# Performance work log

Hardware: AMD Instinct MI355X
Metric: run time of the kernel (lower is better)

## Reference

```python
import jax, jax.numpy as jnp
import numpy as np

STRIDE = 1
MAX_STRIDE = 250  # 25 * 10 default


def setup_inputs() -> dict:
    key = jax.random.key(0)
    k1, k2 = jax.random.split(key)
    T = 1_000_000
    prediction = jax.random.normal(k1, (T,), dtype=jnp.float32)
    ground_truth = jax.random.normal(k2, (T,), dtype=jnp.float32)
    return {"prediction": prediction, "ground_truth": ground_truth}


def reference(prediction, ground_truth):
    T = prediction.shape[0]
    lags = jnp.arange(0, MAX_STRIDE, STRIDE)
    idx = jnp.arange(T)

    # ground-truth statistics are lag-independent
    mean_gt = jnp.mean(ground_truth)
    var_gt = jnp.var(ground_truth, ddof=1)  # torch.var is unbiased
    v_gt = ground_truth - mean_gt

    def ccc_at_lag(n):
        # shifted pred: n leading zeros followed by prediction[:-n]
        src = idx - n
        pred = jnp.where(src >= 0, prediction[jnp.clip(src, 0)], 0.0)
        mean_pred = jnp.mean(pred)
        var_pred = jnp.var(pred, ddof=1)
        cov = jnp.mean((pred - mean_pred) * v_gt)  # population covariance
        denom = var_gt + var_pred + (mean_gt - mean_pred) ** 2
        return 2.0 * cov / denom

    cccs = jax.vmap(ccc_at_lag)(lags)  # [n_lags]
    return 1.0 - jnp.mean(cccs)
```

## Files before the change

kernel.cpp:

```cpp
#include <hip/hip_runtime.h>
#include <hip/hip_bf16.h>


#define TC 2048
#define NLAG 256
#define NUSED 250
#define GT4 (TC / 4 + 66)
#define STATS_OFF (512 * NLAG)
#define STATS_PITCH 512

__device__ __forceinline__ float4 ld_gt_sw(const float* s_gt, int i4) {
    int s = i4 ^ ((i4 >> 3) & 7);
    return *(const float4*)&s_gt[4 * s];
}

__global__ __launch_bounds__(256) void ccc_main(const float* __restrict__ pred,
                                                const float* __restrict__ gt,
                                                float* __restrict__ ws, int T) {
    __shared__ __align__(16) float s_pred[TC];
    __shared__ __align__(16) float s_gt[GT4 * 4];
    __shared__ __align__(16) float s_acc[8][NLAG];
    __shared__ float s_red[4][4];

    const int tid = threadIdx.x;
    const int c = blockIdx.x;
    const int j0 = c * TC;

    float sp = 0.f, qp = 0.f, sg = 0.f, qg = 0.f;
    #pragma unroll 2
    for (int i4 = tid; i4 < TC / 4; i4 += 256) {
        int g = j0 + 4 * i4;
        float4 v = make_float4(0.f, 0.f, 0.f, 0.f);
        if (g + 3 < T) v = *(const float4*)&pred[g];
        *(float4*)&s_pred[4 * i4] = v;
        sp += v.x + v.y + v.z + v.w;
        qp += v.x * v.x + v.y * v.y + v.z * v.z + v.w * v.w;
    }
    #pragma unroll 2
    for (int i4 = tid; i4 < GT4; i4 += 256) {
        int g = j0 + 4 * i4;
        float4 v = make_float4(0.f, 0.f, 0.f, 0.f);
        if (g + 3 < T) v = *(const float4*)&gt[g];
        int s = i4 ^ ((i4 >> 3) & 7);
        *(float4*)&s_gt[4 * s] = v;
        if (i4 < TC / 4) {
            sg += v.x + v.y + v.z + v.w;
            qg += v.x * v.x + v.y * v.y + v.z * v.z + v.w * v.w;
        }
    }
    __syncthreads();

    const int sub = tid >> 5;
    const int l = tid & 31;
    int gi = sub * 64 + 2 * l;
    const int pi0 = sub * 64;

    float w[12];
    {
        float4 a = ld_gt_sw(s_gt, gi);
        float4 b = ld_gt_sw(s_gt, gi + 1);
        float4 d = ld_gt_sw(s_gt, gi + 2);
        w[0] = a.x; w[1] = a.y; w[2] = a.z; w[3] = a.w;
        w[4] = b.x; w[5] = b.y; w[6] = b.z; w[7] = b.w;
        w[8] = d.x; w[9] = d.y; w[10] = d.z; w[11] = d.w;
    }
    float acc[8] = {0.f, 0.f, 0.f, 0.f, 0.f, 0.f, 0.f, 0.f};

    #pragma unroll 4
    for (int it = 0; it < 64; ++it) {
        float4 nw = ld_gt_sw(s_gt, gi + 3 + it);
        float4 p = *(const float4*)&s_pred[4 * (pi0 + it)];
        #pragma unroll
        for (int k = 0; k < 8; ++k) {
            acc[k] = fmaf(p.x, w[k], acc[k]);
            acc[k] = fmaf(p.y, w[k + 1], acc[k]);
            acc[k] = fmaf(p.z, w[k + 2], acc[k]);
            acc[k] = fmaf(p.w, w[k + 3], acc[k]);
        }
        #pragma unroll
        for (int i = 0; i < 8; ++i) w[i] = w[i + 4];
        w[8] = nw.x; w[9] = nw.y; w[10] = nw.z; w[11] = nw.w;
    }

    const int wv = tid >> 6, ln = tid & 63;
    #pragma unroll
    for (int off = 32; off > 0; off >>= 1) {
        sp += __shfl_down(sp, off, 64);
        qp += __shfl_down(qp, off, 64);
        sg += __shfl_down(sg, off, 64);
        qg += __shfl_down(qg, off, 64);
    }
    if (ln == 0) { s_red[wv][0] = sp; s_red[wv][1] = qp; s_red[wv][2] = sg; s_red[wv][3] = qg; }

    #pragma unroll
    for (int k = 0; k < 8; ++k) s_acc[sub][8 * l + k] = acc[k];
    __syncthreads();

    float lagsum = 0.f;
    #pragma unroll
    for (int s = 0; s < 8; ++s) lagsum += s_acc[s][tid];
    ws[c * NLAG + tid] = lagsum;

    if (tid < 4) {
        ws[STATS_OFF + tid * STATS_PITCH + c] =
            s_red[0][tid] + s_red[1][tid] + s_red[2][tid] + s_red[3][tid];
    }
}

__global__ __launch_bounds__(1024) void ccc_finalize(const float* __restrict__ pred,
                                                     const float* __restrict__ ws,
                                                     float* __restrict__ out, int T, int nch) {
    __shared__ float s_part[4][NLAG];
    __shared__ float s_stats[4];
    __shared__ float s_tail[NLAG];
    __shared__ float s_sum[NLAG];

    const int t = threadIdx.x;
    const int q = t >> 8, lag = t & 255;

    float sum = 0.f;
    #pragma unroll 4
    for (int c = q; c < nch; c += 4) sum += ws[c * NLAG + lag];
    s_part[q][lag] = sum;

    if (t < 256) {
        int st = t >> 6, ln = t & 63;
        float s = 0.f;
        for (int c = ln; c < nch; c += 64) s += ws[STATS_OFF + st * STATS_PITCH + c];
        #pragma unroll
        for (int off = 32; off > 0; off >>= 1) s += __shfl_down(s, off, 64);
        if (ln == 0) s_stats[st] = s;
        int g = T - NLAG + t;
        s_tail[t] = (g >= 0 && g < T) ? pred[g] : 0.f;
    }
    __syncthreads();

    if (t < 256) {
        float lagC = s_part[0][t] + s_part[1][t] + s_part[2][t] + s_part[3][t];
        float v = 0.f;
        if (t < NUSED) {
            const float Tf = (float)T;
            float sum_pred = s_stats[0], sumsq_pred = s_stats[1];
            float sum_gt = s_stats[2], sumsq_gt = s_stats[3];
            float mean_gt = sum_gt / Tf;
            float var_gt = (sumsq_gt - sum_gt * sum_gt / Tf) / (Tf - 1.f);
            float tail_s = 0.f, tail_q = 0.f;
            for (int i = 1; i <= t; ++i) {
                float x = s_tail[NLAG - i];
                tail_s += x; tail_q += x * x;
            }
            float S = sum_pred - tail_s;
            float Q = sumsq_pred - tail_q;
            float mean_p = S / Tf;
            float var_p = (Q - S * S / Tf) / (Tf - 1.f);
            float cov = (lagC - mean_gt * S) / Tf;
            float dm = mean_gt - mean_p;
            v = 2.f * cov / (var_gt + var_p + dm * dm);
        }
        s_sum[t] = v;
    }
    __syncthreads();
    for (int s = 128; s > 0; s >>= 1) {
        if (t < s) s_sum[t] += s_sum[t + s];
        __syncthreads();
    }
    if (t == 0) out[0] = 1.f - s_sum[0] / (float)NUSED;
}

extern "C" void kernel_launch(void* const* d_in, const int* in_sizes, int n_in,
                              void* d_out, int out_size, void* d_ws, size_t ws_size,
                              hipStream_t stream) {
    const float* pred = (const float*)d_in[0];
    const float* gt   = (const float*)d_in[1];
    float* out = (float*)d_out;
    float* ws  = (float*)d_ws;
    const int T = in_sizes[0];
    const int nch = (T + TC - 1) / TC;

    ccc_main<<<nch, 256, 0, stream>>>(pred, gt, ws, T);
    ccc_finalize<<<1, 1024, 0, stream>>>(pred, ws, out, T, nch);
}
```

Before: 84.95 us.

## Parallelize finalize reduction with scan-based tail sums and vectorized partial loads

The finalize kernel now replaces the per-lag serial tail summation (up to 250 iterations per thread) with a Hillis-Steele suffix scan over the last 256 predictions. It sums per-chunk lag partials using float4 loads across 16 waves. Per-chunk statistics are stored interleaved with a stride of 32 floats per chunk, and the main correlation loop unroll goes from 4 to 8. The scan adds eight barrier rounds, and the tail load no longer bounds-checks for T < 256.

```diff
diff --git a/kernel.cpp b/kernel.cpp
--- a/kernel.cpp
+++ b/kernel.cpp
@@ -6,8 +6,7 @@
 #define NLAG 256
 #define NUSED 250
 #define GT4 (TC / 4 + 66)
-#define STATS_OFF (512 * NLAG)
-#define STATS_PITCH 512
+#define STAT_OFF (512 * NLAG)
 
 __device__ __forceinline__ float4 ld_gt_sw(const float* s_gt, int i4) {
     int s = i4 ^ ((i4 >> 3) & 7);
@@ -66,7 +65,7 @@
     }
     float acc[8] = {0.f, 0.f, 0.f, 0.f, 0.f, 0.f, 0.f, 0.f};
 
-    #pragma unroll 4
+    #pragma unroll 8
     for (int it = 0; it < 64; ++it) {
         float4 nw = ld_gt_sw(s_gt, gi + 3 + it);
         float4 p = *(const float4*)&s_pred[4 * (pi0 + it)];
@@ -100,9 +99,8 @@
     #pragma unroll
     for (int s = 0; s < 8; ++s) lagsum += s_acc[s][tid];
     ws[c * NLAG + tid] = lagsum;
-
     if (tid < 4) {
-        ws[STATS_OFF + tid * STATS_PITCH + c] =
+        ws[STAT_OFF + 32 * c + tid] =
             s_red[0][tid] + s_red[1][tid] + s_red[2][tid] + s_red[3][tid];
     }
 }
@@ -110,33 +108,57 @@
 __global__ __launch_bounds__(1024) void ccc_finalize(const float* __restrict__ pred,
                                                      const float* __restrict__ ws,
                                                      float* __restrict__ out, int T, int nch) {
-    __shared__ float s_part[4][NLAG];
+    __shared__ __align__(16) float s_p4[16 * NLAG];
+    __shared__ float s_tail[NLAG];
+    __shared__ float s_sa[NLAG], s_sb[NLAG], s_qa[NLAG], s_qb[NLAG];
+    __shared__ float s_fin[NLAG];
     __shared__ float s_stats[4];
-    __shared__ float s_tail[NLAG];
-    __shared__ float s_sum[NLAG];
 
     const int t = threadIdx.x;
-    const int q = t >> 8, lag = t & 255;
-
-    float sum = 0.f;
-    #pragma unroll 4
-    for (int c = q; c < nch; c += 4) sum += ws[c * NLAG + lag];
-    s_part[q][lag] = sum;
+    const int wv = t >> 6, ln = t & 63;
+
+    if (t < NLAG) {
+        float x = pred[T - NLAG + t];
+        s_tail[t] = x;
+        s_sa[t] = x;
+        s_qa[t] = x * x;
+    }
+
+    {
+        float4 a = make_float4(0.f, 0.f, 0.f, 0.f);
+        #pragma unroll 8
+        for (int c = wv; c < nch; c += 16) {
+            float4 v = *(const float4*)&ws[c * NLAG + 4 * ln];
+            a.x += v.x; a.y += v.y; a.z += v.z; a.w += v.w;
+        }
+        *(float4*)&s_p4[wv * NLAG + 4 * ln] = a;
+    }
 
     if (t < 256) {
-        int st = t >> 6, ln = t & 63;
+        int st = t >> 6;
         float s = 0.f;
-        for (int c = ln; c < nch; c += 64) s += ws[STATS_OFF + st * STATS_PITCH + c];
+        for (int cc = ln; cc < nch; cc += 64) s += ws[STAT_OFF + 32 * cc + st];
         #pragma unroll
         for (int off = 32; off > 0; off >>= 1) s += __shfl_down(s, off, 64);
         if (ln == 0) s_stats[st] = s;
-        int g = T - NLAG + t;
-        s_tail[t] = (g >= 0 && g < T) ? pred[g] : 0.f;
-    }
-    __syncthreads();
-
-    if (t < 256) {
-        float lagC = s_part[0][t] + s_part[1][t] + s_part[2][t] + s_part[3][t];
+    }
+    __syncthreads();
+
+    float *sa = s_sa, *sb = s_sb, *qa = s_qa, *qb = s_qb;
+    for (int d = 1; d < NLAG; d <<= 1) {
+        if (t < NLAG) {
+            sb[t] = sa[t] + ((t + d < NLAG) ? sa[t + d] : 0.f);
+            qb[t] = qa[t] + ((t + d < NLAG) ? qa[t + d] : 0.f);
+        }
+        __syncthreads();
+        float* tmp = sa; sa = sb; sb = tmp;
+        tmp = qa; qa = qb; qb = tmp;
+    }
+
+    if (t < NLAG) {
+        float lagC = 0.f;
+        #pragma unroll
+        for (int w = 0; w < 16; ++w) lagC += s_p4[w * NLAG + t];
         float v = 0.f;
         if (t < NUSED) {
             const float Tf = (float)T;
@@ -144,11 +166,8 @@
             float sum_gt = s_stats[2], sumsq_gt = s_stats[3];
             float mean_gt = sum_gt / Tf;
             float var_gt = (sumsq_gt - sum_gt * sum_gt / Tf) / (Tf - 1.f);
-            float tail_s = 0.f, tail_q = 0.f;
-            for (int i = 1; i <= t; ++i) {
-                float x = s_tail[NLAG - i];
-                tail_s += x; tail_q += x * x;
-            }
+            float tail_s = (t == 0) ? 0.f : sa[NLAG - t];
+            float tail_q = (t == 0) ? 0.f : qa[NLAG - t];
             float S = sum_pred - tail_s;
             float Q = sumsq_pred - tail_q;
             float mean_p = S / Tf;
@@ -157,14 +176,14 @@
             float dm = mean_gt - mean_p;
             v = 2.f * cov / (var_gt + var_p + dm * dm);
         }
-        s_sum[t] = v;
+        s_fin[t] = v;
     }
     __syncthreads();
     for (int s = 128; s > 0; s >>= 1) {
-        if (t < s) s_sum[t] += s_sum[t + s];
+        if (t < s) s_fin[t] += s_fin[t + s];
         __syncthreads();
     }
-    if (t == 0) out[0] = 1.f - s_sum[0] / (float)NUSED;
+    if (t == 0) out[0] = 1.f - s_fin[0] / (float)NUSED;
 }
 
 extern "C" void kernel_launch(void* const* d_in, const int* in_sizes, int n_in,
```

After: 77.30 us. -9.0%, faster.
